# Optimization experiments

Measured on AMD Instinct MI355X. Metric: run time of the kernel, lower is better.

The kernel has to match this reference:

```python
import jax, jax.numpy as jnp
import numpy as np

INNER_DIM = 64
NEG = 1e12


def _rotate_half_interleaved(x):
    # stack([-x[..., 1::2], x[..., ::2]], -1).reshape(x.shape)
    x2 = jnp.stack([-x[..., 1::2], x[..., ::2]], axis=-1)
    return x2.reshape(x.shape)


def setup_inputs() -> dict:
    key = jax.random.key(0)
    k1, k2 = jax.random.split(key)
    B, S, H = 16, 512, 768
    T, D = 9, INNER_DIM
    hidden = jax.random.normal(k1, (B, S, H), dtype=jnp.float32)
    W = jax.random.normal(k2, (H, T * 2 * D), dtype=jnp.float32) * 0.02
    b = jnp.zeros((T * 2 * D,), dtype=jnp.float32)
    attention_mask = jnp.ones((B, S), dtype=jnp.int32)
    return {"hidden": hidden, "W": W, "b": b, "attention_mask": attention_mask}


def reference(hidden, W, b, attention_mask):
    B, S, H = hidden.shape
    D = INNER_DIM
    T = W.shape[1] // (2 * D)

    # dense + split into per-type q/k: [B, S, T, 2D]
    out = (jnp.einsum('bsh,hc->bsc', hidden, W) + b).reshape(B, S, T, 2 * D)
    qw, kw = out[..., :D], out[..., D:]

    # inline sinusoidal RoPE (interleaved sin/cos layout)
    pos = jnp.arange(S, dtype=jnp.float32)[:, None]            # [S, 1]
    inv = jnp.power(10000.0, -2.0 * jnp.arange(D // 2, dtype=jnp.float32) / D)
    ang = pos * inv                                            # [S, D/2]
    cos_pos = jnp.repeat(jnp.cos(ang), 2, axis=-1)[None, :, None, :]  # [1,S,1,D]
    sin_pos = jnp.repeat(jnp.sin(ang), 2, axis=-1)[None, :, None, :]
    qw = qw * cos_pos + _rotate_half_interleaved(qw) * sin_pos
    kw = kw * cos_pos + _rotate_half_interleaved(kw) * sin_pos

    # pairwise scores per entity type: [B, T, S, S]
    logits = jnp.einsum('bmtd,bntd->btmn', qw, kw)

    # padding mask (key dim only, as in original expand) with large negative
    pm = attention_mask.astype(logits.dtype)[:, None, None, :]  # [B,1,1,S]
    logits = logits * pm - (1.0 - pm) * NEG

    # strict lower-triangular mask (only upper-triangular spans valid)
    tril = jnp.tril(jnp.ones((S, S), dtype=logits.dtype), -1)
    logits = logits - tril * NEG

    return logits / np.sqrt(D).astype(np.float32)
```

## Files before the change

kernel.cpp:

```cpp
#include <hip/hip_runtime.h>
#include <cstdint>
#include <cstddef>

#define NEG_C 1000000000000.0f

typedef __bf16 bf16x8 __attribute__((ext_vector_type(8)));
typedef float f32x4 __attribute__((ext_vector_type(4)));

union Frag {
    int4 i;
    bf16x8 b;
};

__device__ __forceinline__ unsigned short f32_to_bf16_rne(float f) {
    unsigned int u = __float_as_uint(f);
    u += 0x7fffu + ((u >> 16) & 1u);
    return (unsigned short)(u >> 16);
}

__device__ __forceinline__ void async_copy16(const void* g, void* l) {
    __builtin_amdgcn_global_load_lds(
        (const __attribute__((address_space(1))) unsigned int*)(uintptr_t)g,
        (__attribute__((address_space(3))) unsigned int*)(uintptr_t)l,
        16, 0, 0);
}

__global__ void convert_hidden_kernel(const float* __restrict__ src,
                                      unsigned short* __restrict__ dst, int n4) {
    int idx = blockIdx.x * blockDim.x + threadIdx.x;
    if (idx >= n4) return;
    float4 v = ((const float4*)src)[idx];
    ushort4 o;
    o.x = f32_to_bf16_rne(v.x);
    o.y = f32_to_bf16_rne(v.y);
    o.z = f32_to_bf16_rne(v.z);
    o.w = f32_to_bf16_rne(v.w);
    ((ushort4*)dst)[idx] = o;
}

__global__ void transpose_w_kernel(const float* __restrict__ W,
                                   unsigned short* __restrict__ WT) {
    __shared__ unsigned short tile[32][33];
    int bx = blockIdx.x;
    int by = blockIdx.y;
    int x = threadIdx.x & 31;
    int y0 = threadIdx.x >> 5;
#pragma unroll
    for (int yy = 0; yy < 32; yy += 8) {
        int k = by * 32 + y0 + yy;
        int n = bx * 32 + x;
        tile[y0 + yy][x] = f32_to_bf16_rne(W[(size_t)k * 1152 + n]);
    }
    __syncthreads();
#pragma unroll
    for (int yy = 0; yy < 32; yy += 8) {
        int n = bx * 32 + y0 + yy;
        int k = by * 32 + x;
        WT[(size_t)n * 768 + k] = tile[x][y0 + yy];
    }
}

__global__ __launch_bounds__(256, 2) void gemm1_kernel(
    const unsigned short* __restrict__ Ah, const unsigned short* __restrict__ WT,
    const float* __restrict__ bias, unsigned short* __restrict__ proj) {
    const int K = 768, N = 1152;
    __shared__ unsigned short As[128 * 64];
    __shared__ unsigned short Bs[128 * 64];
    int tid = threadIdx.x;
    int lane = tid & 63;
    int wave = tid >> 6;
    int bm = blockIdx.x * 128;
    int bn = blockIdx.y * 128;
    int wm = (wave & 1) * 64;
    int wn = (wave >> 1) * 64;
    int col_l = lane & 15;
    int qg = lane >> 4;

    int c0 = wave * 4 * 64 + lane;
    f32x4 acc[4][4] = {};

    for (int k0 = 0; k0 < K; k0 += 64) {
        __syncthreads();
#pragma unroll
        for (int q = 0; q < 4; ++q) {
            int c = c0 + q * 64;
            int r = c >> 3;
            int g = (c & 7) ^ (r & 7);
            async_copy16(Ah + (size_t)(bm + r) * K + k0 + g * 8,
                         As + (size_t)(wave * 4 + q) * 512);
            async_copy16(WT + (size_t)(bn + r) * K + k0 + g * 8,
                         Bs + (size_t)(wave * 4 + q) * 512);
        }
        __syncthreads();
#pragma unroll
        for (int ks = 0; ks < 2; ++ks) {
            Frag qf[4], kf[4];
            int g = ks * 4 + qg;
#pragma unroll
            for (int i = 0; i < 4; ++i) {
                int rm = wm + i * 16 + col_l;
                int rn = wn + i * 16 + col_l;
                qf[i].i = *(const int4*)(As + rm * 64 + ((g ^ (rm & 7)) * 8));
                kf[i].i = *(const int4*)(Bs + rn * 64 + ((g ^ (rn & 7)) * 8));
            }
#pragma unroll
            for (int i = 0; i < 4; ++i)
#pragma unroll
                for (int j = 0; j < 4; ++j)
                    acc[i][j] = __builtin_amdgcn_mfma_f32_16x16x32_bf16(
                        kf[i].b, qf[j].b, acc[i][j], 0, 0, 0);
        }
    }

#pragma unroll
    for (int i = 0; i < 4; ++i) {
        int cn0 = wn + i * 16 + qg * 4;
        int gn0 = bn + cn0;
        float4 bb = *(const float4*)(bias + gn0);
        int p0 = cn0 >> 1;
        float inv0 = exp2f(-0.41524101186091903f * (float)p0);
        float inv1 = exp2f(-0.41524101186091903f * (float)(p0 + 1));
#pragma unroll
        for (int j = 0; j < 4; ++j) {
            int gm = bm + wm + j * 16 + col_l;
            float s = (float)(gm & 511);
            float a0 = s * inv0, a1 = s * inv1;
            float sn0 = __sinf(a0), cs0 = __cosf(a0);
            float sn1 = __sinf(a1), cs1 = __cosf(a1);
            float v0 = acc[i][j][0] + bb.x;
            float v1 = acc[i][j][1] + bb.y;
            float v2 = acc[i][j][2] + bb.z;
            float v3 = acc[i][j][3] + bb.w;
            ushort4 o;
            o.x = f32_to_bf16_rne(v0 * cs0 - v1 * sn0);
            o.y = f32_to_bf16_rne(v1 * cs0 + v0 * sn0);
            o.z = f32_to_bf16_rne(v2 * cs1 - v3 * sn1);
            o.w = f32_to_bf16_rne(v3 * cs1 + v2 * sn1);
            *(ushort4*)(proj + (size_t)gm * N + gn0) = o;
        }
    }
}

__global__ __launch_bounds__(256, 2) void gemm2_kernel(
    const unsigned short* __restrict__ proj, const int* __restrict__ mask,
    float* __restrict__ out) {
    __shared__ unsigned short Qs[128 * 64];
    __shared__ unsigned short Ks[128 * 64];
    int bid = blockIdx.x;
    int batch = bid >> 4;
    int tl = bid & 15;
    int tm = tl >> 2, tn = tl & 3;
    int b = batch / 9, t = batch - b * 9;
    int tid = threadIdx.x, lane = tid & 63, wave = tid >> 6;
    int wm = (wave & 1) * 64, wn = (wave >> 1) * 64;
    int col_l = lane & 15;
    int qg = lane >> 4;
    size_t out_base = ((size_t)b * 9 + t) * 512 * 512;

    if (tm > tn) {
#pragma unroll 4
        for (int r = 0; r < 128; r += 8) {
            int row = r + (tid >> 5);
            int c4 = (tid & 31) * 4;
            int gm = tm * 128 + row;
            int gn = tn * 128 + c4;
            int4 mi = *(const int4*)(mask + b * 512 + gn);
            f32x4 v;
            v[0] = (-(1.0f - (float)mi.x) * NEG_C - NEG_C) * 0.125f;
            v[1] = (-(1.0f - (float)mi.y) * NEG_C - NEG_C) * 0.125f;
            v[2] = (-(1.0f - (float)mi.z) * NEG_C - NEG_C) * 0.125f;
            v[3] = (-(1.0f - (float)mi.w) * NEG_C - NEG_C) * 0.125f;
            __builtin_nontemporal_store(v, (f32x4*)(out + out_base + (size_t)gm * 512 + gn));
        }
        return;
    }

    const unsigned short* qbase = proj + (((size_t)(b * 512 + tm * 128) * 9) + t) * 128;
    const unsigned short* kbase = proj + (((size_t)(b * 512 + tn * 128) * 9) + t) * 128 + 64;
#pragma unroll
    for (int q = 0; q < 4; ++q) {
        int c = (wave * 4 + q) * 64 + lane;
        int r = c >> 3;
        int g = (c & 7) ^ (r & 7);
        async_copy16(qbase + (size_t)r * 1152 + g * 8,
                     Qs + (size_t)(wave * 4 + q) * 512);
        async_copy16(kbase + (size_t)r * 1152 + g * 8,
                     Ks + (size_t)(wave * 4 + q) * 512);
    }
    __syncthreads();

    f32x4 acc[4][4] = {};
#pragma unroll
    for (int ks = 0; ks < 2; ++ks) {
        Frag qf[4], kf[4];
        int g = ks * 4 + qg;
#pragma unroll
        for (int i = 0; i < 4; ++i) {
            int rm = wm + i * 16 + col_l;
            int rn = wn + i * 16 + col_l;
            qf[i].i = *(const int4*)(Qs + rm * 64 + ((g ^ (rm & 7)) * 8));
            kf[i].i = *(const int4*)(Ks + rn * 64 + ((g ^ (rn & 7)) * 8));
        }
#pragma unroll
        for (int i = 0; i < 4; ++i)
#pragma unroll
            for (int j = 0; j < 4; ++j)
                acc[i][j] = __builtin_amdgcn_mfma_f32_16x16x32_bf16(
                    kf[i].b, qf[j].b, acc[i][j], 0, 0, 0);
    }

#pragma unroll
    for (int i = 0; i < 4; ++i) {
        int gn0 = tn * 128 + wn + i * 16 + qg * 4;
        int4 mi = *(const int4*)(mask + b * 512 + gn0);
#pragma unroll
        for (int j = 0; j < 4; ++j) {
            int gm = tm * 128 + wm + j * 16 + col_l;
            f32x4 v;
#pragma unroll
            for (int r = 0; r < 4; ++r) {
                float pm = (float)((&mi.x)[r]);
                float x = acc[i][j][r] * pm - (1.0f - pm) * NEG_C;
                if (gm > gn0 + r) x -= NEG_C;
                v[r] = x * 0.125f;
            }
            __builtin_nontemporal_store(v, (f32x4*)(out + out_base + (size_t)gm * 512 + gn0));
        }
    }
}

extern "C" void kernel_launch(void* const* d_in, const int* in_sizes, int n_in,
                              void* d_out, int out_size, void* d_ws, size_t ws_size,
                              hipStream_t stream) {
    const float* hidden = (const float*)d_in[0];
    const float* W      = (const float*)d_in[1];
    const float* bias   = (const float*)d_in[2];
    const int*   mask   = (const int*)d_in[3];
    float* out = (float*)d_out;

    char* ws = (char*)d_ws;
    unsigned short* Ah   = (unsigned short*)(ws);
    unsigned short* WT   = (unsigned short*)(ws + 12582912);
    unsigned short* proj = (unsigned short*)(ws + 14352384);

    convert_hidden_kernel<<<6144, 256, 0, stream>>>(hidden, Ah, 1572864);
    dim3 gt(36, 24);
    transpose_w_kernel<<<gt, 256, 0, stream>>>(W, WT);
    dim3 g1(64, 9);
    gemm1_kernel<<<g1, 256, 0, stream>>>(Ah, WT, bias, proj);
    gemm2_kernel<<<2304, 256, 0, stream>>>(proj, mask, out);
}
```

Baseline: 219.0 us.

## Merge prep kernels, swap gemm1 grid order, raise occupancy, use regular stores

```diff
diff --git a/kernel.cpp b/kernel.cpp
--- a/kernel.cpp
+++ b/kernel.cpp
@@ -25,42 +25,43 @@
         16, 0, 0);
 }
 
-__global__ void convert_hidden_kernel(const float* __restrict__ src,
-                                      unsigned short* __restrict__ dst, int n4) {
-    int idx = blockIdx.x * blockDim.x + threadIdx.x;
-    if (idx >= n4) return;
-    float4 v = ((const float4*)src)[idx];
-    ushort4 o;
-    o.x = f32_to_bf16_rne(v.x);
-    o.y = f32_to_bf16_rne(v.y);
-    o.z = f32_to_bf16_rne(v.z);
-    o.w = f32_to_bf16_rne(v.w);
-    ((ushort4*)dst)[idx] = o;
-}
-
-__global__ void transpose_w_kernel(const float* __restrict__ W,
-                                   unsigned short* __restrict__ WT) {
+__global__ void prep_kernel(const float* __restrict__ W,
+                            unsigned short* __restrict__ WT,
+                            const float* __restrict__ hidden,
+                            unsigned short* __restrict__ Ah) {
     __shared__ unsigned short tile[32][33];
-    int bx = blockIdx.x;
-    int by = blockIdx.y;
-    int x = threadIdx.x & 31;
-    int y0 = threadIdx.x >> 5;
-#pragma unroll
-    for (int yy = 0; yy < 32; yy += 8) {
-        int k = by * 32 + y0 + yy;
-        int n = bx * 32 + x;
-        tile[y0 + yy][x] = f32_to_bf16_rne(W[(size_t)k * 1152 + n]);
-    }
-    __syncthreads();
-#pragma unroll
-    for (int yy = 0; yy < 32; yy += 8) {
-        int n = bx * 32 + y0 + yy;
-        int k = by * 32 + x;
-        WT[(size_t)n * 768 + k] = tile[x][y0 + yy];
-    }
-}
-
-__global__ __launch_bounds__(256, 2) void gemm1_kernel(
+    int blk = blockIdx.x;
+    if (blk < 864) {
+        int bx = blk % 36;
+        int by = blk / 36;
+        int x = threadIdx.x & 31;
+        int y0 = threadIdx.x >> 5;
+#pragma unroll
+        for (int yy = 0; yy < 32; yy += 8) {
+            int k = by * 32 + y0 + yy;
+            int n = bx * 32 + x;
+            tile[y0 + yy][x] = f32_to_bf16_rne(W[(size_t)k * 1152 + n]);
+        }
+        __syncthreads();
+#pragma unroll
+        for (int yy = 0; yy < 32; yy += 8) {
+            int n = bx * 32 + y0 + yy;
+            int k = by * 32 + x;
+            WT[(size_t)n * 768 + k] = tile[x][y0 + yy];
+        }
+    } else {
+        int idx = (blk - 864) * 256 + threadIdx.x;
+        float4 v = ((const float4*)hidden)[idx];
+        ushort4 o;
+        o.x = f32_to_bf16_rne(v.x);
+        o.y = f32_to_bf16_rne(v.y);
+        o.z = f32_to_bf16_rne(v.z);
+        o.w = f32_to_bf16_rne(v.w);
+        ((ushort4*)Ah)[idx] = o;
+    }
+}
+
+__global__ __launch_bounds__(256, 3) void gemm1_kernel(
     const unsigned short* __restrict__ Ah, const unsigned short* __restrict__ WT,
     const float* __restrict__ bias, unsigned short* __restrict__ proj) {
     const int K = 768, N = 1152;
@@ -69,8 +70,8 @@
     int tid = threadIdx.x;
     int lane = tid & 63;
     int wave = tid >> 6;
-    int bm = blockIdx.x * 128;
-    int bn = blockIdx.y * 128;
+    int bm = blockIdx.y * 128;
+    int bn = blockIdx.x * 128;
     int wm = (wave & 1) * 64;
     int wn = (wave >> 1) * 64;
     int col_l = lane & 15;
@@ -117,7 +118,7 @@
         int cn0 = wn + i * 16 + qg * 4;
         int gn0 = bn + cn0;
         float4 bb = *(const float4*)(bias + gn0);
-        int p0 = cn0 >> 1;
+        int p0 = (cn0 & 63) >> 1;
         float inv0 = exp2f(-0.41524101186091903f * (float)p0);
         float inv1 = exp2f(-0.41524101186091903f * (float)(p0 + 1));
 #pragma unroll
@@ -141,7 +142,7 @@
     }
 }
 
-__global__ __launch_bounds__(256, 2) void gemm2_kernel(
+__global__ __launch_bounds__(256, 3) void gemm2_kernel(
     const unsigned short* __restrict__ proj, const int* __restrict__ mask,
     float* __restrict__ out) {
     __shared__ unsigned short Qs[128 * 64];
@@ -170,7 +171,7 @@
             v[1] = (-(1.0f - (float)mi.y) * NEG_C - NEG_C) * 0.125f;
             v[2] = (-(1.0f - (float)mi.z) * NEG_C - NEG_C) * 0.125f;
             v[3] = (-(1.0f - (float)mi.w) * NEG_C - NEG_C) * 0.125f;
-            __builtin_nontemporal_store(v, (f32x4*)(out + out_base + (size_t)gm * 512 + gn));
+            *(f32x4*)(out + out_base + (size_t)gm * 512 + gn) = v;
         }
         return;
     }
@@ -224,7 +225,7 @@
                 if (gm > gn0 + r) x -= NEG_C;
                 v[r] = x * 0.125f;
             }
-            __builtin_nontemporal_store(v, (f32x4*)(out + out_base + (size_t)gm * 512 + gn0));
+            *(f32x4*)(out + out_base + (size_t)gm * 512 + gn0) = v;
         }
     }
 }
@@ -243,10 +244,8 @@
     unsigned short* WT   = (unsigned short*)(ws + 12582912);
     unsigned short* proj = (unsigned short*)(ws + 14352384);
 
-    convert_hidden_kernel<<<6144, 256, 0, stream>>>(hidden, Ah, 1572864);
-    dim3 gt(36, 24);
-    transpose_w_kernel<<<gt, 256, 0, stream>>>(W, WT);
-    dim3 g1(64, 9);
+    prep_kernel<<<7008, 256, 0, stream>>>(W, WT, hidden, Ah);
+    dim3 g1(9, 64);
     gemm1_kernel<<<g1, 256, 0, stream>>>(Ah, WT, bias, proj);
     gemm2_kernel<<<2304, 256, 0, stream>>>(proj, mask, out);
 }
```

New measurement: 214.4 us. 1.02x faster.
